# Kernel tuning notes

Measured on AMD Instinct MI355X. Metric: run time of the kernel, lower is better.

## Reference

```python
import jax, jax.numpy as jnp
import numpy as np

B, IMG, D, HEADS, L, PC, PF, OUT = 8, 128, 128, 4, 2, 8, 4, 32
HC = IMG // PC; NC = HC * HC          # 16x16 -> 256 coarse tokens
HF = IMG // PF; NF = HF * HF          # 32x32 -> 1024 fine tokens


def _ln(x, g, b):
    m = x.mean(-1, keepdims=True)
    v = x.var(-1, keepdims=True)
    return (x - m) * jax.lax.rsqrt(v + 1e-5) * g + b


def _conv(x, w, b, pad):
    y = jax.lax.conv_general_dilated(x, w, (1, 1), ((pad, pad), (pad, pad)),
                                     dimension_numbers=('NCHW', 'OIHW', 'NCHW'))
    return y + b[None, :, None, None]


def _bilinear_ac(x, oh, ow):  # F.interpolate(mode='bilinear', align_corners=True)
    _, _, H, W = x.shape
    ys = jnp.linspace(0.0, H - 1.0, oh)
    xs = jnp.linspace(0.0, W - 1.0, ow)
    y0 = jnp.floor(ys).astype(jnp.int32); y1 = jnp.minimum(y0 + 1, H - 1); wy = (ys - y0)[:, None]
    x0 = jnp.floor(xs).astype(jnp.int32); x1 = jnp.minimum(x0 + 1, W - 1); wx = (xs - x0)[None, :]
    g = lambda yi, xi: x[:, :, yi][:, :, :, xi]
    return (g(y0, x0) * (1 - wy) * (1 - wx) + g(y0, x1) * (1 - wy) * wx
            + g(y1, x0) * wy * (1 - wx) + g(y1, x1) * wy * wx)


def _patchify(x, p):  # F.unfold with kernel=stride=p, in_chans=1
    b, _, h, w = x.shape
    return x.reshape(b, h // p, p, w // p, p).transpose(0, 1, 3, 2, 4).reshape(b, (h // p) * (w // p), p * p)


def _forward(x, Wpc, bpc, Wpf, bpf, type_embed, ln1_g, ln1_b, Wqkv, Wo, bo,
             ln2_g, ln2_b, W1, b1, W2, b2, dWc, dbc, dWf, dbf, fW1, fb1, fW2, fb2):
    Bx = x.shape[0]
    # ---- multi-scale patch embed ----
    coarse = _patchify(x, PC) @ Wpc + bpc + type_embed[0]   # [B,NC,D]
    fine = _patchify(x, PF) @ Wpf + bpf                     # [B,NF,D]
    # ---- edge map: sobel -> avgpool(4) -> threshold at per-image mean ----
    gray = x.mean(1, keepdims=True)
    kx = jnp.array([[[[-1, 0, 1], [-2, 0, 2], [-1, 0, 1]]]], x.dtype)
    ky = jnp.array([[[[-1, -2, -1], [0, 0, 0], [1, 2, 1]]]], x.dtype)
    sx = _conv(gray, kx, jnp.zeros((1,), x.dtype), 1)
    sy = _conv(gray, ky, jnp.zeros((1,), x.dtype), 1)
    e = jnp.sqrt(sx ** 2 + sy ** 2)
    e = e.reshape(Bx, 1, IMG // 4, 4, IMG // 4, 4).mean((3, 5))  # [B,1,32,32] == fine grid
    mask_flat = (e > e.mean((2, 3), keepdims=True)).reshape(Bx, NF)
    # ---- static-shape analogue of per-sample masked gather + pad_sequence:
    # stable sort puts edge tokens first (original pixel order preserved), pads are zeros
    order = jnp.argsort(jnp.logical_not(mask_flat), axis=1, stable=True)   # [B,NF]
    mask_sorted = jnp.take_along_axis(mask_flat, order, 1)
    fine_sorted = jnp.take_along_axis(fine, order[..., None], 1) * mask_sorted[..., None]
    fine_sorted = fine_sorted + type_embed[1]   # type embed added to pads too (as in torch)
    tokens = jnp.concatenate([coarse, fine_sorted], axis=1)   # [B,N,D]
    N = NC + NF
    hd = D // HEADS
    scale = hd ** -0.5
    # ---- encoder blocks (pre-LN attn + MLP, irregular-token path) ----
    for l in range(L):
        y = _ln(tokens, ln1_g[l], ln1_b[l])
        qkv = (y @ Wqkv[l]).reshape(Bx, N, 3, HEADS, hd).transpose(2, 0, 3, 1, 4)
        q, k, v = qkv[0], qkv[1], qkv[2]
        attn = jax.nn.softmax(jnp.einsum('bhqd,bhkd->bhqk', q, k) * scale, axis=-1)
        o = jnp.einsum('bhqk,bhkd->bhqd', attn, v).transpose(0, 2, 1, 3).reshape(Bx, N, D)
        tokens = tokens + o @ Wo[l] + bo[l]
        y = _ln(tokens, ln2_g[l], ln2_b[l])
        tokens = tokens + jax.nn.gelu(y @ W1[l] + b1[l], approximate=False) @ W2[l] + b2[l]
    # ---- multi-scale decoder ----
    c = (tokens[:, :NC] @ dWc + dbc).reshape(Bx, HC, HC, 1).transpose(0, 3, 1, 2)
    c_up = _bilinear_ac(c, OUT, OUT)
    feats = (tokens[:, NC:] @ dWf + dbf) * mask_sorted[..., None]   # pads stay zero
    inv = jnp.argsort(order, axis=1)                                # scatter back to pixel order
    f_flat = jnp.take_along_axis(feats, inv[..., None], 1)          # [B,NF,1]
    f_map = f_flat.reshape(Bx, HF, HF, 1).transpose(0, 3, 1, 2)
    f_up = _bilinear_ac(f_map, OUT, OUT)
    fused = jnp.concatenate([c_up, f_up], axis=1)
    h = jax.nn.relu(_conv(fused, fW1, fb1, 1))
    return _conv(h, fW2, fb2, 1)   # [B,1,32,32]


def setup_inputs() -> dict:
    key = jax.random.key(0)
    ks = jax.random.split(key, 16)
    n = lambda k, shape: jax.random.normal(k, shape, jnp.float32) * 0.02
    z = lambda *shape: jnp.zeros(shape, jnp.float32)
    return {
        'x': jax.random.normal(ks[0], (B, 1, IMG, IMG), jnp.float32),
        'Wpc': n(ks[1], (PC * PC, D)), 'bpc': z(D),
        'Wpf': n(ks[2], (PF * PF, D)), 'bpf': z(D),
        'type_embed': n(ks[3], (2, D)),
        'ln1_g': jnp.ones((L, D), jnp.float32), 'ln1_b': z(L, D),
        'Wqkv': n(ks[4], (L, D, 3 * D)),
        'Wo': n(ks[5], (L, D, D)), 'bo': z(L, D),
        'ln2_g': jnp.ones((L, D), jnp.float32), 'ln2_b': z(L, D),
        'W1': n(ks[6], (L, D, 2 * D)), 'b1': z(L, 2 * D),
        'W2': n(ks[7], (L, 2 * D, D)), 'b2': z(L, D),
        'dWc': n(ks[8], (D, 1)), 'dbc': z(1),
        'dWf': n(ks[9], (D, 1)), 'dbf': z(1),
        'fW1': n(ks[10], (2, 2, 3, 3)) * 10.0, 'fb1': z(2),
        'fW2': n(ks[11], (1, 2, 3, 3)) * 10.0, 'fb2': z(1),
    }


def reference(x, Wpc, bpc, Wpf, bpf, type_embed, ln1_g, ln1_b, Wqkv, Wo, bo,
              ln2_g, ln2_b, W1, b1, W2, b2, dWc, dbc, dWf, dbf, fW1, fb1, fW2, fb2):
    return _forward(x, Wpc, bpc, Wpf, bpf, type_embed, ln1_g, ln1_b, Wqkv, Wo, bo,
                    ln2_g, ln2_b, W1, b1, W2, b2, dWc, dbc, dWf, dbf, fW1, fb1, fW2, fb2)
```

## Files before the change

### kernel.cpp

```cpp
#include <hip/hip_runtime.h>
#include <math.h>

#define Bx 8
#define IMG 128
#define DD 128
#define HEADS 4
#define LL 2
#define PCc 8
#define PFf 4
#define HCc 16
#define NCc 256
#define HFf 32
#define NFf 1024
#define NTOK 1280
#define HD 32
#define SPLIT 4
#define NQT 20

typedef __attribute__((ext_vector_type(8))) short short8;
typedef __attribute__((ext_vector_type(4))) float f32x4;

__device__ __forceinline__ short f2bf(float f) {
  unsigned u = __builtin_bit_cast(unsigned, f);
  u += 0x7FFF + ((u >> 16) & 1);
  return (short)(u >> 16);
}
__device__ __forceinline__ float bf2f(short s) {
  unsigned u = ((unsigned)(unsigned short)s) << 16;
  return __builtin_bit_cast(float, u);
}

__global__ __launch_bounds__(256) void k_prologue(const float* __restrict__ x,
    const float* __restrict__ Wpc, const float* __restrict__ bpc,
    const float* __restrict__ Wpf, const float* __restrict__ bpf,
    const float* __restrict__ te,
    const float* __restrict__ Wqkv, const float* __restrict__ Wo,
    const float* __restrict__ W1, const float* __restrict__ W2,
    short* __restrict__ WtQKV, short* __restrict__ WtO,
    short* __restrict__ Wt1, short* __restrict__ Wt2,
    float* __restrict__ e, float* __restrict__ tokens,
    float* __restrict__ fineb) {
  int blk = blockIdx.x;
  int t = threadIdx.x;
  if (blk < 1024) {
    int idx = blk * 256 + t;
    int l = idx / 131072, r = idx % 131072;
    const float* src; short* dst; int N, off;
    if (r < 49152)      { src = Wqkv + l * 49152; dst = WtQKV + l * 49152; N = 384; off = r; }
    else if (r < 65536) { src = Wo + l * 16384;  dst = WtO + l * 16384;  N = 128; off = r - 49152; }
    else if (r < 98304) { src = W1 + l * 32768;  dst = Wt1 + l * 32768;  N = 256; off = r - 65536; }
    else                { src = W2 + l * 32768;  dst = Wt2 + l * 32768;  N = 128; off = r - 98304; }
    int k = off / N, n = off % N;
    int K = (r >= 98304) ? 256 : 128;
    dst[(size_t)n * K + k] = f2bf(src[off]);
  } else if (blk < 1536) {
    int bt = blk - 1024;
    int b = bt >> 6, tile = bt & 63;
    int ty = tile >> 3, tx = tile & 7;
    int ly = t >> 4, lx = t & 15;
    int py = ty * 16 + ly, px = tx * 16 + lx;
    const float* img = x + (size_t)b * IMG * IMG;
    float v[3][3];
    #pragma unroll
    for (int ky = 0; ky < 3; ++ky)
      #pragma unroll
      for (int kx = 0; kx < 3; ++kx) {
        int yy = py + ky - 1, xx = px + kx - 1;
        v[ky][kx] = (yy >= 0 && yy < IMG && xx >= 0 && xx < IMG)
                        ? img[yy * IMG + xx] : 0.f;
      }
    float gx = -v[0][0] + v[0][2] - 2.f * v[1][0] + 2.f * v[1][2] - v[2][0] + v[2][2];
    float gy = -v[0][0] - 2.f * v[0][1] - v[0][2] + v[2][0] + 2.f * v[2][1] + v[2][2];
    __shared__ float sm[256];
    sm[t] = sqrtf(gx * gx + gy * gy);
    __syncthreads();
    if (t < 16) {
      int cy = t >> 2, cx = t & 3;
      float s = 0.f;
      #pragma unroll
      for (int dy = 0; dy < 4; ++dy)
        #pragma unroll
        for (int dx = 0; dx < 4; ++dx) s += sm[(cy * 4 + dy) * 16 + cx * 4 + dx];
      e[b * NFf + (ty * 4 + cy) * 32 + tx * 4 + cx] = s * (1.f / 16.f);
    }
  } else if (blk < 2560) {
    int bt = (blk - 1536) * 2 + (t >> 7);
    int b = bt / NCc, tok = bt % NCc;
    int hc = tok / HCc, wc = tok % HCc;
    int half = t >> 7, d = t & 127;
    __shared__ float patch[2][PCc * PCc];
    if (d < PCc * PCc) {
      int pi = d / PCc, pj = d % PCc;
      patch[half][d] = x[(b * IMG + hc * PCc + pi) * IMG + wc * PCc + pj];
    }
    __syncthreads();
    float acc = bpc[d] + te[d];
    #pragma unroll 8
    for (int i = 0; i < PCc * PCc; ++i) acc += patch[half][i] * Wpc[i * DD + d];
    tokens[(size_t)(b * NTOK + tok) * DD + d] = acc;
  } else {
    int ft = (blk - 2560) * 2 + (t >> 7);
    int b = ft >> 10, tloc = ft & 1023;
    int hf = tloc >> 5, wf = tloc & 31;
    int half = t >> 7, d = t & 127;
    __shared__ float patch[2][PFf * PFf];
    if (d < PFf * PFf) {
      int pi = d / PFf, pj = d % PFf;
      patch[half][d] = x[(b * IMG + hf * PFf + pi) * IMG + wf * PFf + pj];
    }
    __syncthreads();
    float acc = bpf[d];
    #pragma unroll
    for (int i = 0; i < PFf * PFf; ++i) acc += patch[half][i] * Wpf[i * DD + d];
    fineb[(size_t)(b * NFf + tloc) * DD + d] = acc;
  }
}

__global__ __launch_bounds__(1024) void k_edge_sort(const float* __restrict__ e,
    int* __restrict__ order, float* __restrict__ msort) {
  int b = blockIdx.x;
  int t = threadIdx.x;
  int lane = t & 63, wave = t >> 6;
  float ev = e[b * NFf + t];
  __shared__ float wsum[16];
  __shared__ int wcnt[16];
  float r = ev;
  #pragma unroll
  for (int o = 32; o > 0; o >>= 1) r += __shfl_xor(r, o, 64);
  if (lane == 0) wsum[wave] = r;
  __syncthreads();
  float tot = 0.f;
  #pragma unroll
  for (int i = 0; i < 16; ++i) tot += wsum[i];
  float mean = tot * (1.f / 1024.f);
  int m = (ev > mean) ? 1 : 0;
  unsigned long long bal = __ballot(m);
  if (lane == 0) wcnt[wave] = __popcll(bal);
  __syncthreads();
  int wbase = 0, total = 0;
  #pragma unroll
  for (int i = 0; i < 16; ++i) {
    int c = wcnt[i];
    if (i < wave) wbase += c;
    total += c;
  }
  unsigned long long below = (lane == 63) ? ~0ULL : ((1ULL << (lane + 1)) - 1);
  int incl = __popcll(bal & below);
  int eb = wbase + incl - m;
  int pos = m ? eb : (total + t - eb);
  order[b * NFf + pos] = t;
  msort[b * NFf + pos] = (float)m;
}

__global__ __launch_bounds__(256) void k_gather_qkv(float* __restrict__ tokens,
    const float* __restrict__ fineb, const int* __restrict__ order,
    const float* __restrict__ msort, const float* __restrict__ te,
    const float* __restrict__ g, const float* __restrict__ bb,
    const short* __restrict__ WtQ, short* __restrict__ qkvb) {
  __shared__ short Blds[128 * 128];
  __shared__ short Ylds[32 * 136];
  int row0 = blockIdx.x * 32;
  int t = threadIdx.x;
  int lane = t & 63, w = t >> 6;
  int m = lane & 15, quad = lane >> 4;
  int rt = w >> 1, ch = w & 1;
  int lrow = lane >> 4, jphys = lane & 15;
  f32x4 zero = {0.f, 0.f, 0.f, 0.f};

  #pragma unroll
  for (int j = 0; j < 8; ++j) {
    int c = j * 4 + w;
    int r = c * 4 + lrow;
    int jlog = jphys ^ (r & 15);
    __builtin_amdgcn_global_load_lds(
        (const unsigned*)&WtQ[(size_t)r * 128 + jlog * 8],
        (unsigned*)&Blds[c * 512], 16, 0, 0);
  }
  float2 gg = ((const float2*)g)[lane];
  float2 bv = ((const float2*)bb)[lane];
  #pragma unroll
  for (int rr = 0; rr < 8; ++rr) {
    int lr = w * 8 + rr;
    int row = row0 + lr;
    int b = row / NTOK, rl = row % NTOK;
    float2 v;
    if (rl < NCc) {
      v = ((const float2*)(tokens + (size_t)row * DD))[lane];
    } else {
      int pos = rl - NCc;
      int src = order[b * NFf + pos];
      float mk = msort[b * NFf + pos];
      float2 u = ((const float2*)(fineb + (size_t)(b * NFf + src) * DD))[lane];
      float2 tv = ((const float2*)(te + DD))[lane];
      v.x = u.x * mk + tv.x;
      v.y = u.y * mk + tv.y;
      ((float2*)(tokens + (size_t)row * DD))[lane] = v;
    }
    float s = v.x + v.y;
    #pragma unroll
    for (int o = 32; o > 0; o >>= 1) s += __shfl_xor(s, o, 64);
    float mean = s * (1.f / 128.f);
    float cx = v.x - mean, cy = v.y - mean;
    float q = cx * cx + cy * cy;
    #pragma unroll
    for (int o = 32; o > 0; o >>= 1) q += __shfl_xor(q, o, 64);
    float rstd = rsqrtf(q * (1.f / 128.f) + 1e-5f);
    int p = (int)(unsigned short)f2bf(cx * rstd * gg.x + bv.x)
          | ((int)(unsigned short)f2bf(cy * rstd * gg.y + bv.y) << 16);
    ((int*)Ylds)[lr * 68 + lane] = p;
  }
  for (int c3 = 0; c3 < 3; ++c3) {
    if (c3) {
      __syncthreads();
      #pragma unroll
      for (int j = 0; j < 8; ++j) {
        int c = j * 4 + w;
        int r = c * 4 + lrow;
        int jlog = jphys ^ (r & 15);
        __builtin_amdgcn_global_load_lds(
            (const unsigned*)&WtQ[(size_t)(c3 * 128 + r) * 128 + jlog * 8],
            (unsigned*)&Blds[c * 512], 16, 0, 0);
      }
    }
    __syncthreads();
    f32x4 qa[4] = {zero, zero, zero, zero};
    #pragma unroll
    for (int ks = 0; ks < 4; ++ks) {
      short8 af = *(const short8*)&Ylds[(rt * 16 + m) * 136 + quad * 8 + ks * 32];
      int pc = ((quad + ks * 4) ^ m) * 8;
      #pragma unroll
      for (int nt = 0; nt < 4; ++nt) {
        short8 bf = *(const short8*)&Blds[(ch * 64 + nt * 16 + m) * 128 + pc];
        qa[nt] = __builtin_amdgcn_mfma_f32_16x16x32_bf16(af, bf, qa[nt], 0, 0, 0);
      }
    }
    #pragma unroll
    for (int nt = 0; nt < 4; ++nt) {
      int col = c3 * 128 + ch * 64 + nt * 16 + m;
      #pragma unroll
      for (int r = 0; r < 4; ++r) {
        int row = row0 + rt * 16 + quad * 4 + r;
        qkvb[(size_t)row * 384 + col] = f2bf(qa[nt][r]);
      }
    }
  }
}

__global__ __launch_bounds__(256) void k_fused(const short* __restrict__ Opart,
    const float* __restrict__ Lpart, const short* __restrict__ WtO,
    const float* __restrict__ bo_, const float* __restrict__ ln2g_,
    const float* __restrict__ ln2b_, const short* __restrict__ Wt1,
    const float* __restrict__ b1_, const short* __restrict__ Wt2,
    const float* __restrict__ b2_, float* __restrict__ tokens,
    const float* __restrict__ ln1g_, const float* __restrict__ ln1b_,
    const short* __restrict__ WtQ, short* __restrict__ qkvb,
    const float* __restrict__ dWc_, const float* __restrict__ dbc_,
    const float* __restrict__ dWf_, const float* __restrict__ dbf_,
    float* __restrict__ hrow) {
  __shared__ short Blds[128 * 128];
  __shared__ short AH[32 * 268];
  __shared__ short Ylds[32 * 136];
  __shared__ float pls[2][32], plq[2][32];
  int row0 = blockIdx.x * 32;
  int b = row0 / NTOK;
  int rloc = row0 % NTOK;
  int qt = rloc >> 6, qoff = rloc & 63;
  int t = threadIdx.x;
  int lane = t & 63, w = t >> 6;
  int m = lane & 15, quad = lane >> 4;
  int rt = w >> 1, ch = w & 1;
  int lrow = lane >> 4, jphys = lane & 15;
  f32x4 zero = {0.f, 0.f, 0.f, 0.f};

  #pragma unroll
  for (int j = 0; j < 8; ++j) {
    int c = j * 4 + w;
    int r = c * 4 + lrow;
    int jlog = jphys ^ (r & 15);
    __builtin_amdgcn_global_load_lds(
        (const unsigned*)&WtO[(size_t)r * 128 + jlog * 8],
        (unsigned*)&Blds[c * 512], 16, 0, 0);
  }
  #pragma unroll
  for (int it = 0; it < 2; ++it) {
    int idx = t + it * 256;
    int q = idx >> 4, j = idx & 15;
    int dh = j >> 2, dd = (j & 3) * 8;
    int qg = qoff + q;
    size_t pb = ((size_t)(b * HEADS + dh) * NQT + qt) * SPLIT;
    float L = Lpart[(pb + 0) * 64 + qg] + Lpart[(pb + 1) * 64 + qg]
            + Lpart[(pb + 2) * 64 + qg] + Lpart[(pb + 3) * 64 + qg];
    float o[8] = {0, 0, 0, 0, 0, 0, 0, 0};
    #pragma unroll
    for (int sk = 0; sk < SPLIT; ++sk) {
      short8 po = *(const short8*)&Opart[(pb + sk) * 2048 + qg * 32 + dd];
      #pragma unroll
      for (int i = 0; i < 8; ++i) o[i] += bf2f(po[i]);
    }
    float rs = 1.f / L;
    short8 ov;
    #pragma unroll
    for (int i = 0; i < 8; ++i) ov[i] = f2bf(o[i] * rs);
    *(short8*)&AH[q * 136 + j * 8] = ov;
  }
  __syncthreads();
  f32x4 acc[4] = {zero, zero, zero, zero};
  #pragma unroll
  for (int ks = 0; ks < 4; ++ks) {
    short8 af = *(const short8*)&AH[(rt * 16 + m) * 136 + quad * 8 + ks * 32];
    int pc = ((quad + ks * 4) ^ m) * 8;
    #pragma unroll
    for (int nt = 0; nt < 4; ++nt) {
      short8 bf = *(const short8*)&Blds[(ch * 64 + nt * 16 + m) * 128 + pc];
      acc[nt] = __builtin_amdgcn_mfma_f32_16x16x32_bf16(af, bf, acc[nt], 0, 0, 0);
    }
  }
  float v[4][4];
  #pragma unroll
  for (int nt = 0; nt < 4; ++nt) {
    int col = ch * 64 + nt * 16 + m;
    float bv = bo_[col];
    #pragma unroll
    for (int r = 0; r < 4; ++r) {
      int row = row0 + rt * 16 + quad * 4 + r;
      v[nt][r] = acc[nt][r] + bv + tokens[(size_t)row * DD + col];
    }
  }
  #pragma unroll
  for (int r = 0; r < 4; ++r) {
    float s = v[0][r] + v[1][r] + v[2][r] + v[3][r];
    float q = v[0][r] * v[0][r] + v[1][r] * v[1][r]
            + v[2][r] * v[2][r] + v[3][r] * v[3][r];
    #pragma unroll
    for (int o = 1; o < 16; o <<= 1) { s += __shfl_xor(s, o); q += __shfl_xor(q, o); }
    if (m == 0) {
      int lr = rt * 16 + quad * 4 + r;
      pls[ch][lr] = s;
      plq[ch][lr] = q;
    }
  }
  __syncthreads();
  #pragma unroll
  for (int j = 0; j < 8; ++j) {
    int c = j * 4 + w;
    int r = c * 4 + lrow;
    int jlog = jphys ^ (r & 15);
    __builtin_amdgcn_global_load_lds(
        (const unsigned*)&Wt1[(size_t)r * 128 + jlog * 8],
        (unsigned*)&Blds[c * 512], 16, 0, 0);
  }
  #pragma unroll
  for (int r = 0; r < 4; ++r) {
    int lr = rt * 16 + quad * 4 + r;
    float S = pls[0][lr] + pls[1][lr];
    float Q = plq[0][lr] + plq[1][lr];
    float mean = S * (1.f / 128.f);
    float var = Q * (1.f / 128.f) - mean * mean;
    float rstd = rsqrtf(var + 1e-5f);
    #pragma unroll
    for (int nt = 0; nt < 4; ++nt) {
      int col = ch * 64 + nt * 16 + m;
      Ylds[lr * 136 + col] = f2bf((v[nt][r] - mean) * rstd * ln2g_[col] + ln2b_[col]);
    }
  }
  for (int hh = 0; hh < 2; ++hh) {
    if (hh) {
      __syncthreads();
      #pragma unroll
      for (int j = 0; j < 8; ++j) {
        int c = j * 4 + w;
        int r = c * 4 + lrow;
        int jlog = jphys ^ (r & 15);
        __builtin_amdgcn_global_load_lds(
            (const unsigned*)&Wt1[(size_t)(128 + r) * 128 + jlog * 8],
            (unsigned*)&Blds[c * 512], 16, 0, 0);
      }
    }
    __syncthreads();
    f32x4 ha[4] = {zero, zero, zero, zero};
    #pragma unroll
    for (int ks = 0; ks < 4; ++ks) {
      short8 af = *(const short8*)&Ylds[(rt * 16 + m) * 136 + quad * 8 + ks * 32];
      int pc = ((quad + ks * 4) ^ m) * 8;
      #pragma unroll
      for (int nt = 0; nt < 4; ++nt) {
        short8 bf = *(const short8*)&Blds[(ch * 64 + nt * 16 + m) * 128 + pc];
        ha[nt] = __builtin_amdgcn_mfma_f32_16x16x32_bf16(af, bf, ha[nt], 0, 0, 0);
      }
    }
    #pragma unroll
    for (int nt = 0; nt < 4; ++nt) {
      int n = hh * 128 + ch * 64 + nt * 16 + m;
      float bv = b1_[n];
      #pragma unroll
      for (int r = 0; r < 4; ++r) {
        float vv = ha[nt][r] + bv;
        vv = 0.5f * vv * (1.f + erff(vv * 0.70710678118654752f));
        AH[(rt * 16 + quad * 4 + r) * 268 + n] = f2bf(vv);
      }
    }
  }
  f32x4 a2[4] = {zero, zero, zero, zero};
  for (int kb = 0; kb < 2; ++kb) {
    __syncthreads();
    #pragma unroll
    for (int j = 0; j < 8; ++j) {
      int c = j * 4 + w;
      int r = c * 4 + lrow;
      int jlog = jphys ^ (r & 15);
      __builtin_amdgcn_global_load_lds(
          (const unsigned*)&Wt2[(size_t)r * 256 + kb * 128 + jlog * 8],
          (unsigned*)&Blds[c * 512], 16, 0, 0);
    }
    __syncthreads();
    #pragma unroll
    for (int ks = 0; ks < 4; ++ks) {
      int pc = ((quad + ks * 4) ^ m) * 8;
      short8 af = *(const short8*)&AH[(rt * 16 + m) * 268 + kb * 128
                                      + quad * 8 + ks * 32];
      #pragma unroll
      for (int nt = 0; nt < 4; ++nt) {
        short8 bf = *(const short8*)&Blds[(ch * 64 + nt * 16 + m) * 128 + pc];
        a2[nt] = __builtin_amdgcn_mfma_f32_16x16x32_bf16(af, bf, a2[nt], 0, 0, 0);
      }
    }
  }
  #pragma unroll
  for (int nt = 0; nt < 4; ++nt) {
    int col = ch * 64 + nt * 16 + m;
    float bv = b2_[col];
    #pragma unroll
    for (int r = 0; r < 4; ++r) {
      int row = row0 + rt * 16 + quad * 4 + r;
      float val = a2[nt][r] + bv + v[nt][r];
      tokens[(size_t)row * DD + col] = val;
      v[nt][r] = val;
    }
  }
  if (ln1g_ == nullptr) {
    bool coarse = (rloc < NCc);
    const float* dw = coarse ? dWc_ : dWf_;
    float dwv[4];
    #pragma unroll
    for (int nt = 0; nt < 4; ++nt) dwv[nt] = dw[ch * 64 + nt * 16 + m];
    #pragma unroll
    for (int r = 0; r < 4; ++r) {
      float s = v[0][r] * dwv[0] + v[1][r] * dwv[1]
              + v[2][r] * dwv[2] + v[3][r] * dwv[3];
      #pragma unroll
      for (int o = 1; o < 16; o <<= 1) s += __shfl_xor(s, o);
      if (m == 0) pls[ch][rt * 16 + quad * 4 + r] = s;
    }
    __syncthreads();
    if (m == 0 && ch == 0) {
      float dbv = coarse ? dbc_[0] : dbf_[0];
      #pragma unroll
      for (int r = 0; r < 4; ++r) {
        int lr = rt * 16 + quad * 4 + r;
        hrow[row0 + lr] = pls[0][lr] + pls[1][lr] + dbv;
      }
    }
    return;
  }
  #pragma unroll
  for (int r = 0; r < 4; ++r) {
    float s = v[0][r] + v[1][r] + v[2][r] + v[3][r];
    float q = v[0][r] * v[0][r] + v[1][r] * v[1][r]
            + v[2][r] * v[2][r] + v[3][r] * v[3][r];
    #pragma unroll
    for (int o = 1; o < 16; o <<= 1) { s += __shfl_xor(s, o); q += __shfl_xor(q, o); }
    if (m == 0) {
      int lr = rt * 16 + quad * 4 + r;
      pls[ch][lr] = s;
      plq[ch][lr] = q;
    }
  }
  __syncthreads();
  #pragma unroll
  for (int j = 0; j < 8; ++j) {
    int c = j * 4 + w;
    int r = c * 4 + lrow;
    int jlog = jphys ^ (r & 15);
    __builtin_amdgcn_global_load_lds(
        (const unsigned*)&WtQ[(size_t)r * 128 + jlog * 8],
        (unsigned*)&Blds[c * 512], 16, 0, 0);
  }
  #pragma unroll
  for (int r = 0; r < 4; ++r) {
    int lr = rt * 16 + quad * 4 + r;
    float S = pls[0][lr] + pls[1][lr];
    float Q = plq[0][lr] + plq[1][lr];
    float mean = S * (1.f / 128.f);
    float var = Q * (1.f / 128.f) - mean * mean;
    float rstd = rsqrtf(var + 1e-5f);
    #pragma unroll
    for (int nt = 0; nt < 4; ++nt) {
      int col = ch * 64 + nt * 16 + m;
      Ylds[lr * 136 + col] = f2bf((v[nt][r] - mean) * rstd * ln1g_[col] + ln1b_[col]);
    }
  }
  for (int c3 = 0; c3 < 3; ++c3) {
    if (c3) {
      __syncthreads();
      #pragma unroll
      for (int j = 0; j < 8; ++j) {
        int c = j * 4 + w;
        int r = c * 4 + lrow;
        int jlog = jphys ^ (r & 15);
        __builtin_amdgcn_global_load_lds(
            (const unsigned*)&WtQ[(size_t)(c3 * 128 + r) * 128 + jlog * 8],
            (unsigned*)&Blds[c * 512], 16, 0, 0);
      }
    }
    __syncthreads();
    f32x4 qa[4] = {zero, zero, zero, zero};
    #pragma unroll
    for (int ks = 0; ks < 4; ++ks) {
      short8 af = *(const short8*)&Ylds[(rt * 16 + m) * 136 + quad * 8 + ks * 32];
      int pc = ((quad + ks * 4) ^ m) * 8;
      #pragma unroll
      for (int nt = 0; nt < 4; ++nt) {
        short8 bf = *(const short8*)&Blds[(ch * 64 + nt * 16 + m) * 128 + pc];
        qa[nt] = __builtin_amdgcn_mfma_f32_16x16x32_bf16(af, bf, qa[nt], 0, 0, 0);
      }
    }
    #pragma unroll
    for (int nt = 0; nt < 4; ++nt) {
      int col = c3 * 128 + ch * 64 + nt * 16 + m;
      #pragma unroll
      for (int r = 0; r < 4; ++r) {
        int row = row0 + rt * 16 + quad * 4 + r;
        qkvb[(size_t)row * 384 + col] = f2bf(qa[nt][r]);
      }
    }
  }
}

__global__ __launch_bounds__(256) void k_attn4(const short* __restrict__ qkv,
    short* __restrict__ Opart, float* __restrict__ Lpart) {
  __shared__ short Ks[64 * 32];
  __shared__ short Vt[32 * 74];
  __shared__ short Pl[4][16 * 74];

  int sk = blockIdx.x % SPLIT;
  int qt = (blockIdx.x / SPLIT) % NQT;
  int h  = (blockIdx.x / (SPLIT * NQT)) % HEADS;
  int b  = blockIdx.x / (SPLIT * NQT * HEADS);
  int t = threadIdx.x;
  int lane = t & 63, w = t >> 6;
  int m = lane & 15, quad = lane >> 4;
  int q0 = qt * 64 + w * 16;

  const float scale = 0.17677669529663687f;
  short8 qraw = *(const short8*)(qkv + ((size_t)(b * NTOK) + q0 + m) * 384 + h * HD + quad * 8);
  short8 qf;
  #pragma unroll
  for (int j = 0; j < 8; ++j) qf[j] = f2bf(bf2f(qraw[j]) * scale);

  f32x4 zero = {0.f, 0.f, 0.f, 0.f};
  f32x4 Oacc[2] = {zero, zero};
  float psum[4] = {0.f, 0.f, 0.f, 0.f};

  int skey = t >> 2, sdseg = t & 3;
  int jlogK = sdseg ^ ((skey >> 1) & 3);
  const short* kstage = qkv + ((size_t)(b * NTOK) + skey) * 384 + 128 + h * HD + jlogK * 8;
  const short* vstage = qkv + ((size_t)(b * NTOK) + skey) * 384 + 256 + h * HD + sdseg * 8;
  int kswz = (quad ^ ((m >> 1) & 3)) * 8;

  for (int s = sk * 5; s < sk * 5 + 5; ++s) {
    __syncthreads();
    __builtin_amdgcn_global_load_lds((const unsigned*)(kstage + (size_t)s * 64 * 384),
                                     (unsigned*)&Ks[w * 512], 16, 0, 0);
    short8 vf = *(const short8*)(vstage + (size_t)s * 64 * 384);
    #pragma unroll
    for (int j = 0; j < 8; ++j) Vt[(sdseg * 8 + j) * 74 + skey] = vf[j];
    __syncthreads();

    f32x4 sc[4];
    #pragma unroll
    for (int ct = 0; ct < 4; ++ct) {
      short8 kfrag = *(const short8*)&Ks[(ct * 16 + m) * 32 + kswz];
      sc[ct] = __builtin_amdgcn_mfma_f32_16x16x32_bf16(qf, kfrag, zero, 0, 0, 0);
    }
    #pragma unroll
    for (int ct = 0; ct < 4; ++ct)
      #pragma unroll
      for (int r = 0; r < 4; ++r) {
        float p = __expf(sc[ct][r]);
        unsigned u = __builtin_bit_cast(unsigned, p);
        psum[r] += __builtin_bit_cast(float, u & 0xffff0000u);
        Pl[w][(quad * 4 + r) * 74 + ct * 16 + m] = (short)(u >> 16);
      }
    #pragma unroll
    for (int ks = 0; ks < 2; ++ks) {
      short8 pfrag = *(const short8*)&Pl[w][m * 74 + ks * 32 + quad * 8];
      #pragma unroll
      for (int nt = 0; nt < 2; ++nt) {
        short8 vfrag = *(const short8*)&Vt[(nt * 16 + m) * 74 + ks * 32 + quad * 8];
        Oacc[nt] = __builtin_amdgcn_mfma_f32_16x16x32_bf16(pfrag, vfrag, Oacc[nt], 0, 0, 0);
      }
    }
  }
  #pragma unroll
  for (int r = 0; r < 4; ++r) {
    float ssum = psum[r];
    #pragma unroll
    for (int o = 1; o < 16; o <<= 1) ssum += __shfl_xor(ssum, o);
    int qloc = w * 16 + quad * 4 + r;
    #pragma unroll
    for (int nt = 0; nt < 2; ++nt)
      Opart[(size_t)blockIdx.x * 2048 + qloc * 32 + nt * 16 + m] = f2bf(Oacc[nt][r]);
    if (m == 0) Lpart[(size_t)blockIdx.x * 64 + qloc] = ssum;
  }
}

__global__ __launch_bounds__(1024) void k_decoder(const float* __restrict__ hrow,
    const float* __restrict__ msort, const int* __restrict__ order,
    const float* __restrict__ fW1, const float* __restrict__ fb1,
    const float* __restrict__ fW2, const float* __restrict__ fb2,
    float* __restrict__ outp) {
  int b = blockIdx.x;
  int t = threadIdx.x;
  __shared__ float cmap[NCc];
  __shared__ float fmap[1024];
  __shared__ float cup[1024];
  __shared__ float hb[2][1024];
  fmap[order[b * NFf + t]] = hrow[b * NTOK + NCc + t] * msort[b * NFf + t];
  if (t < NCc) cmap[t] = hrow[b * NTOK + t];
  __syncthreads();
  int y = t >> 5, x = t & 31;
  {
    float ys = y * (15.f / 31.f);
    float xs = x * (15.f / 31.f);
    int y0 = (int)floorf(ys); int y1 = min(y0 + 1, 15); float wy = ys - (float)y0;
    int x0 = (int)floorf(xs); int x1 = min(x0 + 1, 15); float wx = xs - (float)x0;
    cup[t] = cmap[y0 * 16 + x0] * (1.f - wy) * (1.f - wx)
           + cmap[y0 * 16 + x1] * (1.f - wy) * wx
           + cmap[y1 * 16 + x0] * wy * (1.f - wx)
           + cmap[y1 * 16 + x1] * wy * wx;
  }
  __syncthreads();
  for (int oc = 0; oc < 2; ++oc) {
    float a = fb1[oc];
    #pragma unroll
    for (int ic = 0; ic < 2; ++ic)
      #pragma unroll
      for (int ky = 0; ky < 3; ++ky)
        #pragma unroll
        for (int kx = 0; kx < 3; ++kx) {
          int yy = y + ky - 1, xx = x + kx - 1;
          float v = 0.f;
          if (yy >= 0 && yy < 32 && xx >= 0 && xx < 32)
            v = ic == 0 ? cup[yy * 32 + xx] : fmap[yy * 32 + xx];
          a += v * fW1[((oc * 2 + ic) * 3 + ky) * 3 + kx];
        }
    hb[oc][t] = fmaxf(a, 0.f);
  }
  __syncthreads();
  float a = fb2[0];
  #pragma unroll
  for (int ic = 0; ic < 2; ++ic)
    #pragma unroll
    for (int ky = 0; ky < 3; ++ky)
      #pragma unroll
      for (int kx = 0; kx < 3; ++kx) {
        int yy = y + ky - 1, xx = x + kx - 1;
        float v = (yy >= 0 && yy < 32 && xx >= 0 && xx < 32)
                      ? hb[ic][yy * 32 + xx] : 0.f;
        a += v * fW2[(ic * 3 + ky) * 3 + kx];
      }
  outp[b * 1024 + t] = a;
}

extern "C" void kernel_launch(void* const* d_in, const int* in_sizes, int n_in,
                              void* d_out, int out_size, void* d_ws, size_t ws_size,
                              hipStream_t stream) {
  const float* x    = (const float*)d_in[0];
  const float* Wpc  = (const float*)d_in[1];
  const float* bpc  = (const float*)d_in[2];
  const float* Wpf  = (const float*)d_in[3];
  const float* bpf  = (const float*)d_in[4];
  const float* te   = (const float*)d_in[5];
  const float* ln1g = (const float*)d_in[6];
  const float* ln1b = (const float*)d_in[7];
  const float* Wqkv = (const float*)d_in[8];
  const float* Wo   = (const float*)d_in[9];
  const float* bo   = (const float*)d_in[10];
  const float* ln2g = (const float*)d_in[11];
  const float* ln2b = (const float*)d_in[12];
  const float* W1   = (const float*)d_in[13];
  const float* b1   = (const float*)d_in[14];
  const float* W2   = (const float*)d_in[15];
  const float* b2   = (const float*)d_in[16];
  const float* dWc  = (const float*)d_in[17];
  const float* dbc  = (const float*)d_in[18];
  const float* dWf  = (const float*)d_in[19];
  const float* dbf  = (const float*)d_in[20];
  const float* fW1  = (const float*)d_in[21];
  const float* fb1  = (const float*)d_in[22];
  const float* fW2  = (const float*)d_in[23];
  const float* fb2  = (const float*)d_in[24];

  char* ws = (char*)d_ws;
  float* tokens = (float*)ws;                 ws += 1310720 * 4;
  float* fineb  = (float*)ws;                 ws += 1048576 * 4;
  short* qkvb   = (short*)ws;                 ws += 3932160 * 2;
  short* Opart  = (short*)ws;                 ws += (size_t)(Bx * HEADS * NQT * SPLIT) * 2048 * 2;
  float* Lpart  = (float*)ws;                 ws += (size_t)(Bx * HEADS * NQT * SPLIT) * 64 * 4;
  short* WtQKV  = (short*)ws;                 ws += 98304 * 2;
  short* WtO    = (short*)ws;                 ws += 32768 * 2;
  short* Wt1    = (short*)ws;                 ws += 65536 * 2;
  short* Wt2    = (short*)ws;                 ws += 65536 * 2;
  float* ebuf   = (float*)ws;                 ws += 8192 * 4;
  float* msort  = (float*)ws;                 ws += 8192 * 4;
  int*   order  = (int*)ws;                   ws += 8192 * 4;
  float* hrow   = (float*)ws;                 ws += 10240 * 4;

  const int M = Bx * NTOK;

  k_prologue<<<6656, 256, 0, stream>>>(x, Wpc, bpc, Wpf, bpf, te, Wqkv, Wo, W1, W2,
                                       WtQKV, WtO, Wt1, Wt2, ebuf, tokens, fineb);
  k_edge_sort<<<Bx, 1024, 0, stream>>>(ebuf, order, msort);
  k_gather_qkv<<<M / 32, 256, 0, stream>>>(tokens, fineb, order, msort, te,
                                           ln1g, ln1b, WtQKV, qkvb);

  k_attn4<<<Bx * HEADS * NQT * SPLIT, 256, 0, stream>>>(qkvb, Opart, Lpart);
  k_fused<<<M / 32, 256, 0, stream>>>(
      Opart, Lpart, WtO, bo, ln2g, ln2b,
      Wt1, b1, Wt2, b2, tokens,
      ln1g + DD, ln1b + DD, WtQKV + 49152, qkvb,
      nullptr, nullptr, nullptr, nullptr, nullptr);

  k_attn4<<<Bx * HEADS * NQT * SPLIT, 256, 0, stream>>>(qkvb, Opart, Lpart);
  k_fused<<<M / 32, 256, 0, stream>>>(
      Opart, Lpart, WtO + 16384, bo + DD, ln2g + DD, ln2b + DD,
      Wt1 + 32768, b1 + 256, Wt2 + 32768, b2 + DD, tokens,
      nullptr, nullptr, nullptr, nullptr,
      dWc, dbc, dWf, dbf, hrow);

  k_decoder<<<Bx, 1024, 0, stream>>>(hrow, msort, order,
                                     fW1, fb1, fW2, fb2, (float*)d_out);
}
```

Before: 228.4 us.

## Merge prologue/edge-sort and last fused/decoder via grid barriers; halve attention key split

Fuses the prologue with the edge-mask sort into one persistent kernel, and the final fused layer with the decoder into another. Each pair is joined by a hierarchical atomic grid barrier, which removes two kernel launches and their dependency gaps. It also lowers the attention key split from 4 to 2 with 10 stages per block, cutting partial-result traffic and merge work at the cost of fewer blocks. The grid barriers assume every block is co-resident (768 and 320 blocks), and the barrier counters are zeroed by block 0 inside the same launch, which is a race risk. The decoder now runs with 256 threads per image instead of 1024.

```diff
diff --git a/kernel.cpp b/kernel.cpp
--- a/kernel.cpp
+++ b/kernel.cpp
@@ -14,8 +14,11 @@
 #define NFf 1024
 #define NTOK 1280
 #define HD 32
-#define SPLIT 4
+#define SPLIT 2
+#define NSTG 10
 #define NQT 20
+#define MEGA1_GRID 768
+#define NLEAF 32
 
 typedef __attribute__((ext_vector_type(8))) short short8;
 typedef __attribute__((ext_vector_type(4))) float f32x4;
@@ -30,7 +33,36 @@
   return __builtin_bit_cast(float, u);
 }
 
-__global__ __launch_bounds__(256) void k_prologue(const float* __restrict__ x,
+__device__ __forceinline__ void grid_barrier(int* bar, int nblk) {
+  __syncthreads();
+  if (threadIdx.x == 0) {
+    __threadfence();
+    int g = __hip_atomic_load(&bar[0], __ATOMIC_RELAXED, __HIP_MEMORY_SCOPE_AGENT);
+    int leaf = blockIdx.x & (NLEAF - 1);
+    int v = __hip_atomic_fetch_add(&bar[1 + leaf], 1, __ATOMIC_ACQ_REL,
+                                   __HIP_MEMORY_SCOPE_AGENT);
+    if (v == nblk / NLEAF - 1) {
+      int r = __hip_atomic_fetch_add(&bar[33], 1, __ATOMIC_ACQ_REL,
+                                     __HIP_MEMORY_SCOPE_AGENT);
+      if (r == NLEAF - 1)
+        __hip_atomic_fetch_add(&bar[0], 1, __ATOMIC_RELEASE,
+                               __HIP_MEMORY_SCOPE_AGENT);
+    }
+    while (__hip_atomic_load(&bar[0], __ATOMIC_RELAXED,
+                             __HIP_MEMORY_SCOPE_AGENT) == g)
+      __builtin_amdgcn_s_sleep(2);
+    __builtin_amdgcn_fence(__ATOMIC_ACQUIRE, "agent");
+  }
+  __syncthreads();
+}
+
+__device__ __forceinline__ void bar_init(int* bar) {
+  if (blockIdx.x == 0 && threadIdx.x < 40)
+    __hip_atomic_store(&bar[threadIdx.x], 0, __ATOMIC_RELAXED,
+                       __HIP_MEMORY_SCOPE_AGENT);
+}
+
+__global__ __launch_bounds__(256, 4) void k_mega1(const float* __restrict__ x,
     const float* __restrict__ Wpc, const float* __restrict__ bpc,
     const float* __restrict__ Wpf, const float* __restrict__ bpf,
     const float* __restrict__ te,
@@ -39,117 +71,134 @@
     short* __restrict__ WtQKV, short* __restrict__ WtO,
     short* __restrict__ Wt1, short* __restrict__ Wt2,
     float* __restrict__ e, float* __restrict__ tokens,
-    float* __restrict__ fineb) {
-  int blk = blockIdx.x;
+    float* __restrict__ fineb, int* __restrict__ order,
+    float* __restrict__ msort, int* __restrict__ bars) {
+  __shared__ float sob[256];
+  __shared__ float patc[2][PCc * PCc];
+  __shared__ float patf[2][PFf * PFf];
+  __shared__ float wsumf[4];
+  __shared__ int wtot[4];
+  bar_init(bars);
+  int bid = blockIdx.x;
   int t = threadIdx.x;
-  if (blk < 1024) {
-    int idx = blk * 256 + t;
-    int l = idx / 131072, r = idx % 131072;
-    const float* src; short* dst; int N, off;
-    if (r < 49152)      { src = Wqkv + l * 49152; dst = WtQKV + l * 49152; N = 384; off = r; }
-    else if (r < 65536) { src = Wo + l * 16384;  dst = WtO + l * 16384;  N = 128; off = r - 49152; }
-    else if (r < 98304) { src = W1 + l * 32768;  dst = Wt1 + l * 32768;  N = 256; off = r - 65536; }
-    else                { src = W2 + l * 32768;  dst = Wt2 + l * 32768;  N = 128; off = r - 98304; }
-    int k = off / N, n = off % N;
-    int K = (r >= 98304) ? 256 : 128;
-    dst[(size_t)n * K + k] = f2bf(src[off]);
-  } else if (blk < 1536) {
-    int bt = blk - 1024;
-    int b = bt >> 6, tile = bt & 63;
-    int ty = tile >> 3, tx = tile & 7;
-    int ly = t >> 4, lx = t & 15;
-    int py = ty * 16 + ly, px = tx * 16 + lx;
-    const float* img = x + (size_t)b * IMG * IMG;
-    float v[3][3];
-    #pragma unroll
-    for (int ky = 0; ky < 3; ++ky)
-      #pragma unroll
-      for (int kx = 0; kx < 3; ++kx) {
-        int yy = py + ky - 1, xx = px + kx - 1;
-        v[ky][kx] = (yy >= 0 && yy < IMG && xx >= 0 && xx < IMG)
-                        ? img[yy * IMG + xx] : 0.f;
-      }
-    float gx = -v[0][0] + v[0][2] - 2.f * v[1][0] + 2.f * v[1][2] - v[2][0] + v[2][2];
-    float gy = -v[0][0] - 2.f * v[0][1] - v[0][2] + v[2][0] + 2.f * v[2][1] + v[2][2];
-    __shared__ float sm[256];
-    sm[t] = sqrtf(gx * gx + gy * gy);
-    __syncthreads();
-    if (t < 16) {
-      int cy = t >> 2, cx = t & 3;
-      float s = 0.f;
-      #pragma unroll
-      for (int dy = 0; dy < 4; ++dy)
+
+  for (int vb = bid; vb < 6656; vb += MEGA1_GRID) {
+    __syncthreads();
+    if (vb < 1024) {
+      int idx = vb * 256 + t;
+      int l = idx / 131072, r = idx % 131072;
+      const float* src; short* dst; int N, off;
+      if (r < 49152)      { src = Wqkv + l * 49152; dst = WtQKV + l * 49152; N = 384; off = r; }
+      else if (r < 65536) { src = Wo + l * 16384;  dst = WtO + l * 16384;  N = 128; off = r - 49152; }
+      else if (r < 98304) { src = W1 + l * 32768;  dst = Wt1 + l * 32768;  N = 256; off = r - 65536; }
+      else                { src = W2 + l * 32768;  dst = Wt2 + l * 32768;  N = 128; off = r - 98304; }
+      int k = off / N, n = off % N;
+      int K = (r >= 98304) ? 256 : 128;
+      dst[(size_t)n * K + k] = f2bf(src[off]);
+    } else if (vb < 1536) {
+      int bt = vb - 1024;
+      int b = bt >> 6, tile = bt & 63;
+      int ty = tile >> 3, tx = tile & 7;
+      int ly = t >> 4, lx = t & 15;
+      int py = ty * 16 + ly, px = tx * 16 + lx;
+      const float* img = x + (size_t)b * IMG * IMG;
+      float v[3][3];
+      #pragma unroll
+      for (int ky = 0; ky < 3; ++ky)
         #pragma unroll
-        for (int dx = 0; dx < 4; ++dx) s += sm[(cy * 4 + dy) * 16 + cx * 4 + dx];
-      e[b * NFf + (ty * 4 + cy) * 32 + tx * 4 + cx] = s * (1.f / 16.f);
-    }
-  } else if (blk < 2560) {
-    int bt = (blk - 1536) * 2 + (t >> 7);
-    int b = bt / NCc, tok = bt % NCc;
-    int hc = tok / HCc, wc = tok % HCc;
-    int half = t >> 7, d = t & 127;
-    __shared__ float patch[2][PCc * PCc];
-    if (d < PCc * PCc) {
-      int pi = d / PCc, pj = d % PCc;
-      patch[half][d] = x[(b * IMG + hc * PCc + pi) * IMG + wc * PCc + pj];
-    }
-    __syncthreads();
-    float acc = bpc[d] + te[d];
-    #pragma unroll 8
-    for (int i = 0; i < PCc * PCc; ++i) acc += patch[half][i] * Wpc[i * DD + d];
-    tokens[(size_t)(b * NTOK + tok) * DD + d] = acc;
-  } else {
-    int ft = (blk - 2560) * 2 + (t >> 7);
-    int b = ft >> 10, tloc = ft & 1023;
-    int hf = tloc >> 5, wf = tloc & 31;
-    int half = t >> 7, d = t & 127;
-    __shared__ float patch[2][PFf * PFf];
-    if (d < PFf * PFf) {
-      int pi = d / PFf, pj = d % PFf;
-      patch[half][d] = x[(b * IMG + hf * PFf + pi) * IMG + wf * PFf + pj];
-    }
-    __syncthreads();
-    float acc = bpf[d];
-    #pragma unroll
-    for (int i = 0; i < PFf * PFf; ++i) acc += patch[half][i] * Wpf[i * DD + d];
-    fineb[(size_t)(b * NFf + tloc) * DD + d] = acc;
-  }
-}
-
-__global__ __launch_bounds__(1024) void k_edge_sort(const float* __restrict__ e,
-    int* __restrict__ order, float* __restrict__ msort) {
-  int b = blockIdx.x;
-  int t = threadIdx.x;
-  int lane = t & 63, wave = t >> 6;
-  float ev = e[b * NFf + t];
-  __shared__ float wsum[16];
-  __shared__ int wcnt[16];
-  float r = ev;
-  #pragma unroll
-  for (int o = 32; o > 0; o >>= 1) r += __shfl_xor(r, o, 64);
-  if (lane == 0) wsum[wave] = r;
-  __syncthreads();
-  float tot = 0.f;
-  #pragma unroll
-  for (int i = 0; i < 16; ++i) tot += wsum[i];
-  float mean = tot * (1.f / 1024.f);
-  int m = (ev > mean) ? 1 : 0;
-  unsigned long long bal = __ballot(m);
-  if (lane == 0) wcnt[wave] = __popcll(bal);
-  __syncthreads();
-  int wbase = 0, total = 0;
-  #pragma unroll
-  for (int i = 0; i < 16; ++i) {
-    int c = wcnt[i];
-    if (i < wave) wbase += c;
-    total += c;
-  }
-  unsigned long long below = (lane == 63) ? ~0ULL : ((1ULL << (lane + 1)) - 1);
-  int incl = __popcll(bal & below);
-  int eb = wbase + incl - m;
-  int pos = m ? eb : (total + t - eb);
-  order[b * NFf + pos] = t;
-  msort[b * NFf + pos] = (float)m;
+        for (int kx = 0; kx < 3; ++kx) {
+          int yy = py + ky - 1, xx = px + kx - 1;
+          v[ky][kx] = (yy >= 0 && yy < IMG && xx >= 0 && xx < IMG)
+                          ? img[yy * IMG + xx] : 0.f;
+        }
+      float gx = -v[0][0] + v[0][2] - 2.f * v[1][0] + 2.f * v[1][2] - v[2][0] + v[2][2];
+      float gy = -v[0][0] - 2.f * v[0][1] - v[0][2] + v[2][0] + 2.f * v[2][1] + v[2][2];
+      sob[t] = sqrtf(gx * gx + gy * gy);
+      __syncthreads();
+      if (t < 16) {
+        int cy = t >> 2, cx = t & 3;
+        float s = 0.f;
+        #pragma unroll
+        for (int dy = 0; dy < 4; ++dy)
+          #pragma unroll
+          for (int dx = 0; dx < 4; ++dx) s += sob[(cy * 4 + dy) * 16 + cx * 4 + dx];
+        e[b * NFf + (ty * 4 + cy) * 32 + tx * 4 + cx] = s * (1.f / 16.f);
+      }
+    } else if (vb < 2560) {
+      int bt = (vb - 1536) * 2 + (t >> 7);
+      int b = bt / NCc, tok = bt % NCc;
+      int hc = tok / HCc, wc = tok % HCc;
+      int half = t >> 7, d = t & 127;
+      if (d < PCc * PCc) {
+        int pi = d / PCc, pj = d % PCc;
+        patc[half][d] = x[(b * IMG + hc * PCc + pi) * IMG + wc * PCc + pj];
+      }
+      __syncthreads();
+      float acc = bpc[d] + te[d];
+      #pragma unroll 8
+      for (int i = 0; i < PCc * PCc; ++i) acc += patc[half][i] * Wpc[i * DD + d];
+      tokens[(size_t)(b * NTOK + tok) * DD + d] = acc;
+    } else {
+      int ft = (vb - 2560) * 2 + (t >> 7);
+      int b = ft >> 10, tloc = ft & 1023;
+      int hf = tloc >> 5, wf = tloc & 31;
+      int half = t >> 7, d = t & 127;
+      if (d < PFf * PFf) {
+        int pi = d / PFf, pj = d % PFf;
+        patf[half][d] = x[(b * IMG + hf * PFf + pi) * IMG + wf * PFf + pj];
+      }
+      __syncthreads();
+      float acc = bpf[d];
+      #pragma unroll
+      for (int i = 0; i < PFf * PFf; ++i) acc += patf[half][i] * Wpf[i * DD + d];
+      fineb[(size_t)(b * NFf + tloc) * DD + d] = acc;
+    }
+  }
+
+  grid_barrier(bars, MEGA1_GRID);
+
+  if (bid < 8) {
+    int b = bid;
+    int lane = t & 63, wave = t >> 6;
+    float ev[4]; int mm[4];
+    float s4 = 0.f;
+    #pragma unroll
+    for (int i = 0; i < 4; ++i) { ev[i] = e[b * NFf + t * 4 + i]; s4 += ev[i]; }
+    float r = s4;
+    #pragma unroll
+    for (int o = 32; o > 0; o >>= 1) r += __shfl_xor(r, o, 64);
+    if (lane == 0) wsumf[wave] = r;
+    __syncthreads();
+    float tot = wsumf[0] + wsumf[1] + wsumf[2] + wsumf[3];
+    float mean = tot * (1.f / 1024.f);
+    int mcnt = 0;
+    #pragma unroll
+    for (int i = 0; i < 4; ++i) { mm[i] = (ev[i] > mean) ? 1 : 0; mcnt += mm[i]; }
+    int incl = mcnt;
+    #pragma unroll
+    for (int o = 1; o < 64; o <<= 1) {
+      int u = __shfl_up(incl, o, 64);
+      if (lane >= o) incl += u;
+    }
+    if (lane == 63) wtot[wave] = incl;
+    __syncthreads();
+    int wbase = 0, totE = 0;
+    #pragma unroll
+    for (int i = 0; i < 4; ++i) {
+      int c = wtot[i];
+      if (i < wave) wbase += c;
+      totE += c;
+    }
+    int ebase = wbase + incl - mcnt;
+    #pragma unroll
+    for (int i = 0; i < 4; ++i) {
+      int c = t * 4 + i;
+      int pos = mm[i] ? ebase : (totE + c - ebase);
+      order[b * NFf + pos] = c;
+      msort[b * NFf + pos] = (float)mm[i];
+      ebase += mm[i];
+    }
+  }
 }
 
 __global__ __launch_bounds__(256) void k_gather_qkv(float* __restrict__ tokens,
@@ -246,22 +295,21 @@
   }
 }
 
-__global__ __launch_bounds__(256) void k_fused(const short* __restrict__ Opart,
-    const float* __restrict__ Lpart, const short* __restrict__ WtO,
-    const float* __restrict__ bo_, const float* __restrict__ ln2g_,
-    const float* __restrict__ ln2b_, const short* __restrict__ Wt1,
-    const float* __restrict__ b1_, const short* __restrict__ Wt2,
-    const float* __restrict__ b2_, float* __restrict__ tokens,
-    const float* __restrict__ ln1g_, const float* __restrict__ ln1b_,
-    const short* __restrict__ WtQ, short* __restrict__ qkvb,
-    const float* __restrict__ dWc_, const float* __restrict__ dbc_,
-    const float* __restrict__ dWf_, const float* __restrict__ dbf_,
-    float* __restrict__ hrow) {
+__device__ __forceinline__ void fused_body(int row0,
+    const short* __restrict__ Opart, const float* __restrict__ Lpart,
+    const short* __restrict__ WtO, const float* __restrict__ bo_,
+    const float* __restrict__ ln2g_, const float* __restrict__ ln2b_,
+    const short* __restrict__ Wt1, const float* __restrict__ b1_,
+    const short* __restrict__ Wt2, const float* __restrict__ b2_,
+    float* __restrict__ tokens, const float* __restrict__ ln1g_,
+    const float* __restrict__ ln1b_, const short* __restrict__ WtQ,
+    short* __restrict__ qkvb, const float* __restrict__ dWc_,
+    const float* __restrict__ dbc_, const float* __restrict__ dWf_,
+    const float* __restrict__ dbf_, float* __restrict__ hrow) {
   __shared__ short Blds[128 * 128];
   __shared__ short AH[32 * 268];
   __shared__ short Ylds[32 * 136];
   __shared__ float pls[2][32], plq[2][32];
-  int row0 = blockIdx.x * 32;
   int b = row0 / NTOK;
   int rloc = row0 % NTOK;
   int qt = rloc >> 6, qoff = rloc & 63;
@@ -288,8 +336,9 @@
     int dh = j >> 2, dd = (j & 3) * 8;
     int qg = qoff + q;
     size_t pb = ((size_t)(b * HEADS + dh) * NQT + qt) * SPLIT;
-    float L = Lpart[(pb + 0) * 64 + qg] + Lpart[(pb + 1) * 64 + qg]
-            + Lpart[(pb + 2) * 64 + qg] + Lpart[(pb + 3) * 64 + qg];
+    float L = 0.f;
+    #pragma unroll
+    for (int sk = 0; sk < SPLIT; ++sk) L += Lpart[(pb + sk) * 64 + qg];
     float o[8] = {0, 0, 0, 0, 0, 0, 0, 0};
     #pragma unroll
     for (int sk = 0; sk < SPLIT; ++sk) {
@@ -532,6 +581,108 @@
         int row = row0 + rt * 16 + quad * 4 + r;
         qkvb[(size_t)row * 384 + col] = f2bf(qa[nt][r]);
       }
+    }
+  }
+}
+
+__global__ __launch_bounds__(256) void k_fused(const short* __restrict__ Opart,
+    const float* __restrict__ Lpart, const short* __restrict__ WtO,
+    const float* __restrict__ bo_, const float* __restrict__ ln2g_,
+    const float* __restrict__ ln2b_, const short* __restrict__ Wt1,
+    const float* __restrict__ b1_, const short* __restrict__ Wt2,
+    const float* __restrict__ b2_, float* __restrict__ tokens,
+    const float* __restrict__ ln1g_, const float* __restrict__ ln1b_,
+    const short* __restrict__ WtQ, short* __restrict__ qkvb) {
+  fused_body(blockIdx.x * 32, Opart, Lpart, WtO, bo_, ln2g_, ln2b_,
+             Wt1, b1_, Wt2, b2_, tokens, ln1g_, ln1b_, WtQ, qkvb,
+             nullptr, nullptr, nullptr, nullptr, nullptr);
+}
+
+__global__ __launch_bounds__(256, 2) void k_mega3(const short* __restrict__ Opart,
+    const float* __restrict__ Lpart, const short* __restrict__ WtO,
+    const float* __restrict__ bo_, const float* __restrict__ ln2g_,
+    const float* __restrict__ ln2b_, const short* __restrict__ Wt1,
+    const float* __restrict__ b1_, const short* __restrict__ Wt2,
+    const float* __restrict__ b2_, float* __restrict__ tokens,
+    const float* __restrict__ dWc_, const float* __restrict__ dbc_,
+    const float* __restrict__ dWf_, const float* __restrict__ dbf_,
+    float* __restrict__ hrow, const float* __restrict__ msort,
+    const int* __restrict__ order, const float* __restrict__ fW1,
+    const float* __restrict__ fb1, const float* __restrict__ fW2,
+    const float* __restrict__ fb2, float* __restrict__ outp,
+    int* __restrict__ bars) {
+  bar_init(bars);
+  fused_body(blockIdx.x * 32, Opart, Lpart, WtO, bo_, ln2g_, ln2b_,
+             Wt1, b1_, Wt2, b2_, tokens, nullptr, nullptr, nullptr, nullptr,
+             dWc_, dbc_, dWf_, dbf_, hrow);
+  grid_barrier(bars, 320);
+  if (blockIdx.x < 8) {
+    int b = blockIdx.x;
+    int t = threadIdx.x;
+    __shared__ float cmap[NCc];
+    __shared__ float fmap[1024];
+    __shared__ float cup[1024];
+    __shared__ float hb[2][1024];
+    cmap[t] = hrow[b * NTOK + t];
+    #pragma unroll
+    for (int i = 0; i < 4; ++i) {
+      int c = t + 256 * i;
+      fmap[order[b * NFf + c]] = hrow[b * NTOK + NCc + c] * msort[b * NFf + c];
+    }
+    __syncthreads();
+    #pragma unroll
+    for (int i = 0; i < 4; ++i) {
+      int p = t + 256 * i;
+      int y = p >> 5, x = p & 31;
+      float ys = y * (15.f / 31.f);
+      float xs = x * (15.f / 31.f);
+      int y0 = (int)floorf(ys); int y1 = min(y0 + 1, 15); float wy = ys - (float)y0;
+      int x0 = (int)floorf(xs); int x1 = min(x0 + 1, 15); float wx = xs - (float)x0;
+      cup[p] = cmap[y0 * 16 + x0] * (1.f - wy) * (1.f - wx)
+             + cmap[y0 * 16 + x1] * (1.f - wy) * wx
+             + cmap[y1 * 16 + x0] * wy * (1.f - wx)
+             + cmap[y1 * 16 + x1] * wy * wx;
+    }
+    __syncthreads();
+    #pragma unroll
+    for (int i = 0; i < 4; ++i) {
+      int p = t + 256 * i;
+      int y = p >> 5, x = p & 31;
+      for (int oc = 0; oc < 2; ++oc) {
+        float a = fb1[oc];
+        #pragma unroll
+        for (int ic = 0; ic < 2; ++ic)
+          #pragma unroll
+          for (int ky = 0; ky < 3; ++ky)
+            #pragma unroll
+            for (int kx = 0; kx < 3; ++kx) {
+              int yy = y + ky - 1, xx = x + kx - 1;
+              float vv = 0.f;
+              if (yy >= 0 && yy < 32 && xx >= 0 && xx < 32)
+                vv = ic == 0 ? cup[yy * 32 + xx] : fmap[yy * 32 + xx];
+              a += vv * fW1[((oc * 2 + ic) * 3 + ky) * 3 + kx];
+            }
+        hb[oc][p] = fmaxf(a, 0.f);
+      }
+    }
+    __syncthreads();
+    #pragma unroll
+    for (int i = 0; i < 4; ++i) {
+      int p = t + 256 * i;
+      int y = p >> 5, x = p & 31;
+      float a = fb2[0];
+      #pragma unroll
+      for (int ic = 0; ic < 2; ++ic)
+        #pragma unroll
+        for (int ky = 0; ky < 3; ++ky)
+          #pragma unroll
+          for (int kx = 0; kx < 3; ++kx) {
+            int yy = y + ky - 1, xx = x + kx - 1;
+            float vv = (yy >= 0 && yy < 32 && xx >= 0 && xx < 32)
+                          ? hb[ic][yy * 32 + xx] : 0.f;
+            a += vv * fW2[(ic * 3 + ky) * 3 + kx];
+          }
+      outp[b * 1024 + p] = a;
     }
   }
 }
@@ -567,7 +718,7 @@
   const short* vstage = qkv + ((size_t)(b * NTOK) + skey) * 384 + 256 + h * HD + sdseg * 8;
   int kswz = (quad ^ ((m >> 1) & 3)) * 8;
 
-  for (int s = sk * 5; s < sk * 5 + 5; ++s) {
+  for (int s = sk * NSTG; s < sk * NSTG + NSTG; ++s) {
     __syncthreads();
     __builtin_amdgcn_global_load_lds((const unsigned*)(kstage + (size_t)s * 64 * 384),
                                      (unsigned*)&Ks[w * 512], 16, 0, 0);
@@ -612,64 +763,6 @@
       Opart[(size_t)blockIdx.x * 2048 + qloc * 32 + nt * 16 + m] = f2bf(Oacc[nt][r]);
     if (m == 0) Lpart[(size_t)blockIdx.x * 64 + qloc] = ssum;
   }
-}
-
-__global__ __launch_bounds__(1024) void k_decoder(const float* __restrict__ hrow,
-    const float* __restrict__ msort, const int* __restrict__ order,
-    const float* __restrict__ fW1, const float* __restrict__ fb1,
-    const float* __restrict__ fW2, const float* __restrict__ fb2,
-    float* __restrict__ outp) {
-  int b = blockIdx.x;
-  int t = threadIdx.x;
-  __shared__ float cmap[NCc];
-  __shared__ float fmap[1024];
-  __shared__ float cup[1024];
-  __shared__ float hb[2][1024];
-  fmap[order[b * NFf + t]] = hrow[b * NTOK + NCc + t] * msort[b * NFf + t];
-  if (t < NCc) cmap[t] = hrow[b * NTOK + t];
-  __syncthreads();
-  int y = t >> 5, x = t & 31;
-  {
-    float ys = y * (15.f / 31.f);
-    float xs = x * (15.f / 31.f);
-    int y0 = (int)floorf(ys); int y1 = min(y0 + 1, 15); float wy = ys - (float)y0;
-    int x0 = (int)floorf(xs); int x1 = min(x0 + 1, 15); float wx = xs - (float)x0;
-    cup[t] = cmap[y0 * 16 + x0] * (1.f - wy) * (1.f - wx)
-           + cmap[y0 * 16 + x1] * (1.f - wy) * wx
-           + cmap[y1 * 16 + x0] * wy * (1.f - wx)
-           + cmap[y1 * 16 + x1] * wy * wx;
-  }
-  __syncthreads();
-  for (int oc = 0; oc < 2; ++oc) {
-    float a = fb1[oc];
-    #pragma unroll
-    for (int ic = 0; ic < 2; ++ic)
-      #pragma unroll
-      for (int ky = 0; ky < 3; ++ky)
-        #pragma unroll
-        for (int kx = 0; kx < 3; ++kx) {
-          int yy = y + ky - 1, xx = x + kx - 1;
-          float v = 0.f;
-          if (yy >= 0 && yy < 32 && xx >= 0 && xx < 32)
-            v = ic == 0 ? cup[yy * 32 + xx] : fmap[yy * 32 + xx];
-          a += v * fW1[((oc * 2 + ic) * 3 + ky) * 3 + kx];
-        }
-    hb[oc][t] = fmaxf(a, 0.f);
-  }
-  __syncthreads();
-  float a = fb2[0];
-  #pragma unroll
-  for (int ic = 0; ic < 2; ++ic)
-    #pragma unroll
-    for (int ky = 0; ky < 3; ++ky)
-      #pragma unroll
-      for (int kx = 0; kx < 3; ++kx) {
-        int yy = y + ky - 1, xx = x + kx - 1;
-        float v = (yy >= 0 && yy < 32 && xx >= 0 && xx < 32)
-                      ? hb[ic][yy * 32 + xx] : 0.f;
-        a += v * fW2[(ic * 3 + ky) * 3 + kx];
-      }
-  outp[b * 1024 + t] = a;
 }
 
 extern "C" void kernel_launch(void* const* d_in, const int* in_sizes, int n_in,
@@ -715,12 +808,14 @@
   float* msort  = (float*)ws;                 ws += 8192 * 4;
   int*   order  = (int*)ws;                   ws += 8192 * 4;
   float* hrow   = (float*)ws;                 ws += 10240 * 4;
+  int*   bars   = (int*)ws;                   ws += 128 * 4;
 
   const int M = Bx * NTOK;
 
-  k_prologue<<<6656, 256, 0, stream>>>(x, Wpc, bpc, Wpf, bpf, te, Wqkv, Wo, W1, W2,
-                                       WtQKV, WtO, Wt1, Wt2, ebuf, tokens, fineb);
-  k_edge_sort<<<Bx, 1024, 0, stream>>>(ebuf, order, msort);
+  k_mega1<<<MEGA1_GRID, 256, 0, stream>>>(x, Wpc, bpc, Wpf, bpf, te,
+                                          Wqkv, Wo, W1, W2,
+                                          WtQKV, WtO, Wt1, Wt2,
+                                          ebuf, tokens, fineb, order, msort, bars);
   k_gather_qkv<<<M / 32, 256, 0, stream>>>(tokens, fineb, order, msort, te,
                                            ln1g, ln1b, WtQKV, qkvb);
 
@@ -728,16 +823,12 @@
   k_fused<<<M / 32, 256, 0, stream>>>(
       Opart, Lpart, WtO, bo, ln2g, ln2b,
       Wt1, b1, Wt2, b2, tokens,
-      ln1g + DD, ln1b + DD, WtQKV + 49152, qkvb,
-      nullptr, nullptr, nullptr, nullptr, nullptr);
+      ln1g + DD, ln1b + DD, WtQKV + 49152, qkvb);
 
   k_attn4<<<Bx * HEADS * NQT * SPLIT, 256, 0, stream>>>(qkvb, Opart, Lpart);
-  k_fused<<<M / 32, 256, 0, stream>>>(
+  k_mega3<<<M / 32, 256, 0, stream>>>(
       Opart, Lpart, WtO + 16384, bo + DD, ln2g + DD, ln2b + DD,
       Wt1 + 32768, b1 + 256, Wt2 + 32768, b2 + DD, tokens,
-      nullptr, nullptr, nullptr, nullptr,
-      dWc, dbc, dWf, dbf, hrow);
-
-  k_decoder<<<Bx, 1024, 0, stream>>>(hrow, msort, order,
-                                     fW1, fb1, fW2, fb2, (float*)d_out);
-}
+      dWc, dbc, dWf, dbf, hrow, msort, order,
+      fW1, fb1, fW2, fb2, (float*)d_out, bars + 64);
+}
```

After: 319.6 us. 39.9% more time.
